# Kernel tuning notes

Measured on AMD Instinct MI355X. Metric: run time of the kernel, lower is better.

## Reference

```python
import jax, jax.numpy as jnp
import numpy as np
from jax import lax

N, CIN, COUT, T, V, G, K = 32, 64, 64, 256, 25, 8, 3  # batch, channels, time, joints, groups, subsets
EPS = 1e-5  # BatchNorm eps


def setup_inputs() -> dict:
    key = jax.random.key(0)
    ks = jax.random.split(key, 10)
    x = jax.random.normal(ks[0], (N, CIN, T, V), jnp.float32)
    # DecoupleA param: A reshaped [3,1,V,V] tiled over groups (torch .repeat tiles)
    A0 = jax.random.uniform(ks[1], (K, 1, V, V), jnp.float32)
    DecoupleA = jnp.tile(A0, (1, G, 1, 1))
    W = jax.random.normal(ks[2], (CIN, COUT * K), jnp.float32) * np.float32(np.sqrt(0.5 / (COUT * K)))
    b = jnp.full((1, COUT * K, 1, 1), 1e-6, jnp.float32)
    g0 = 1.0 + 0.1 * jax.random.normal(ks[3], (COUT * K,), jnp.float32)
    b0 = 0.1 * jax.random.normal(ks[4], (COUT * K,), jnp.float32)
    g1 = 1.0 + 0.1 * jax.random.normal(ks[5], (COUT,), jnp.float32)
    b1 = 0.1 * jax.random.normal(ks[6], (COUT,), jnp.float32)
    conv_w = jax.random.normal(ks[7], (COUT, COUT, 9, 1), jnp.float32) * np.float32(np.sqrt(2.0 / (COUT * 9)))
    conv_b = jnp.zeros((COUT,), jnp.float32)
    g2 = 1.0 + 0.1 * jax.random.normal(ks[8], (COUT,), jnp.float32)
    b2 = 0.1 * jax.random.normal(ks[9], (COUT,), jnp.float32)
    return {"x": x, "DecoupleA": DecoupleA, "W": W, "b": b, "g0": g0, "b0": b0,
            "g1": g1, "b1": b1, "conv_w": conv_w, "conv_b": conv_b, "g2": g2, "b2": b2,
            "keep_prob": 1}


def _bn_eval(y, g, be):
    # inference BN with running_mean=0, running_var=1
    return y * (g / jnp.sqrt(1.0 + EPS))[None, :, None, None] + be[None, :, None, None]


def reference(x, DecoupleA, W, b, g0, b0, g1, b1, conv_w, conv_b, g2, b2, keep_prob):
    # ---- unit_gcn ----
    learn_A = jnp.tile(DecoupleA, (1, COUT // G, 1, 1))           # [3, COUT, V, V]
    # norm(): right-multiply by diag((colsum + 0.001)^-1) == scale columns
    invD = 1.0 / (jnp.sum(learn_A, axis=2) + 0.001)               # [3, COUT, V]
    normA = learn_A * invD[:, :, None, :]
    y = jnp.einsum('nctw,cd->ndtw', x, W) + b                     # [N, 3*COUT, T, V]
    y = _bn_eval(y, g0, b0)
    y = y.reshape(N, K, COUT, T, V)
    y = jnp.einsum('nkctv,kcvw->nctw', y, normA)                  # message passing
    y = _bn_eval(y, g1, b1)
    y = jax.nn.relu(y + x)                                        # down = identity (CIN==COUT)
    # ---- unit_tcn (keep_prob==1 -> DropBlocks are identity) ----
    z = lax.conv_general_dilated(y, conv_w, (1, 1), [(4, 4), (0, 0)],
                                 dimension_numbers=('NCHW', 'OIHW', 'NCHW'))
    z = z + conv_b[None, :, None, None]
    z = _bn_eval(z, g2, b2)
    # ---- residual (identity, CIN==COUT, stride=1; skip-DropBlocks identity) ----
    return jax.nn.relu(z + x)
```

## Files before the change

### kernel.cpp

```cpp
#include <hip/hip_runtime.h>
#include <hip/hip_bf16.h>
#include <stdint.h>


typedef const float* fp;
typedef __attribute__((ext_vector_type(8))) short short8;
typedef __attribute__((ext_vector_type(4))) float floatx4;

__device__ __forceinline__ float us2f(unsigned int u){
  union { unsigned int i; float f; } c; c.i = u << 16; return c.f;
}
__device__ __forceinline__ unsigned short f2us(float f){
  __hip_bfloat16 h = __float2bfloat16(f);
  return *reinterpret_cast<unsigned short*>(&h);
}
__device__ __forceinline__ void gload_lds16(const void* g, void* l){
  __builtin_amdgcn_global_load_lds(
      (const __attribute__((address_space(1))) void*)g,
      (__attribute__((address_space(3))) void*)l, 16, 0, 0);
}


__global__ __launch_bounds__(256) void k_prep(
    fp x, fp A, fp W, fp b, fp g0, fp b0, fp g1, fp b1,
    fp cw, fp cb, fp g2, fp b2,
    unsigned short* U, float* biasU, unsigned short* xb,
    float* cbe, unsigned short* cwetb)
{
  int bid = blockIdx.x, tid = threadIdx.x;
  const float inv_s = rsqrtf(1.0f + 1e-5f);
  __shared__ __align__(16) char smemraw[26624];

  if (bid < 1792) {
    int m = bid;
    if (m >= 1600) {
      for (int k = tid; k < 1600; k += 256) U[(long long)m*1600 + k] = 0;
      return;
    }
    float* nAL   = (float*)smemraw;
    float* WeffL = (float*)(smemraw + 512);
    float* cs3   = (float*)(smemraw + 1408);
    int c = m & 63, w = m >> 6, g = c & 7;
    if (tid < 75) {
      int kk = tid / 25, vv = tid % 25;
      nAL[tid] = A[((kk*8 + g)*25 + vv)*25 + w];
    }
    if (tid < 192) {
      int kk = tid >> 6, cin = tid & 63;
      WeffL[tid] = W[cin*192 + kk*64 + c] * (g0[kk*64 + c] * inv_s);
    }
    __syncthreads();
    if (tid < 3) {
      float s = 0.f;
      for (int vv = 0; vv < 25; vv++) s += nAL[tid*25 + vv];
      cs3[tid] = s + 0.001f;
    }
    __syncthreads();
    if (tid < 75) nAL[tid] = nAL[tid] / cs3[tid/25];
    __syncthreads();
    float s1 = g1[c] * inv_s;
    for (int k = tid; k < 1600; k += 256) {
      int cin = k / 25, vv = k - cin*25;
      float acc = WeffL[cin]       * nAL[vv]
                + WeffL[64 + cin]  * nAL[25 + vv]
                + WeffL[128 + cin] * nAL[50 + vv];
      acc *= s1;
      if (cin == c && vv == w) acc += 1.0f;
      U[(long long)m*1600 + k] = f2us(acc);
    }
    if (tid == 0) {
      float acc = 0.f;
      for (int kk = 0; kk < 3; kk++) {
        int d = kk*64 + c;
        float be = b[d] * (g0[d] * inv_s) + b0[d];
        for (int v = 0; v < 25; v++) acc += be * nAL[kk*25 + v];
      }
      biasU[m] = acc * s1 + b1[c];
    }
    return;
  }

  if (bid < 2816) {
    int bxt = bid - 1792;
    int n = bxt >> 5, tb = bxt & 31, t0 = tb*8;
    unsigned short* xs = (unsigned short*)smemraw;
    for (int e4 = tid; e4 < 3200; e4 += 256) {
      int c = e4 / 50, r4 = (e4 - c*50)*4;
      floatx4 xv = *(const floatx4*)(x + (long long)(n*64 + c)*6400 + t0*25 + r4);
      int tt = r4 / 25, v = r4 - tt*25;
      xs[(c*8 + tt)*26 + v] = f2us(xv.x); if (++v == 25){v = 0; tt++;}
      xs[(c*8 + tt)*26 + v] = f2us(xv.y); if (++v == 25){v = 0; tt++;}
      xs[(c*8 + tt)*26 + v] = f2us(xv.z); if (++v == 25){v = 0; tt++;}
      xs[(c*8 + tt)*26 + v] = f2us(xv.w);
    }
    __syncthreads();
    for (int e4 = tid; e4 < 3200; e4 += 256) {
      int base = e4 * 4;
      int tt = base / 1600, q0 = base - tt*1600;
      int c = q0 / 25, v = q0 - c*25;
      ushort4 pk;
      pk.x = xs[(c*8 + tt)*26 + v]; if (++v == 25){v = 0; c++;}
      pk.y = xs[(c*8 + tt)*26 + v]; if (++v == 25){v = 0; c++;}
      pk.z = xs[(c*8 + tt)*26 + v]; if (++v == 25){v = 0; c++;}
      pk.w = xs[(c*8 + tt)*26 + v];
      *(ushort4*)(xb + (long long)(n*256 + t0 + tt)*1600 + q0) = pk;
    }
    return;
  }

  int gid = (bid - 2816)*256 + tid;
  if (gid < 36864) {
    int o = gid / 576, r = gid % 576;
    int j = r / 64, i = r % 64;
    cwetb[gid] = f2us(cw[(o*64+i)*9 + j] * (g2[o] * inv_s));
    return;
  }
  gid -= 36864;
  if (gid < 64) {
    cbe[gid] = cb[gid] * (g2[gid] * inv_s) + b2[gid];
  }
}

__global__ __launch_bounds__(256, 2) void k_gemm(
    const unsigned short* U, const unsigned short* xb, const float* biasU,
    unsigned short* yb)
{
  int bm = blockIdx.x >> 6, bn = blockIdx.x & 63;
  int n = bn >> 1, t0 = (bn & 1) * 128;
  int tid = threadIdx.x, lane = tid & 63, wid = tid >> 6;
  int l15 = lane & 15, grp = lane >> 4;

  __shared__ __align__(16) unsigned short As[256*64];
  __shared__ __align__(16) unsigned short Bs[128*64];

  const unsigned short* gA[8];
  const unsigned short* gB[4];
  unsigned short* lA[8];
  unsigned short* lB[4];
  #pragma unroll
  for (int it = 0; it < 8; it++) {
    int e = it*256 + tid;
    int row = e >> 3, li = e & 7;
    int kcol = (li ^ (row & 7)) * 8;
    gA[it] = U + (long long)(bm*256 + row)*1600 + kcol;
    lA[it] = As + e*8;
  }
  #pragma unroll
  for (int it = 0; it < 4; it++) {
    int e = it*256 + tid;
    int row = e >> 3, li = e & 7;
    int kcol = (li ^ (row & 7)) * 8;
    gB[it] = xb + (long long)(n*256 + t0 + row)*1600 + kcol;
    lB[it] = Bs + e*8;
  }

  floatx4 acc[4][8];
  #pragma unroll
  for (int i = 0; i < 4; i++)
    #pragma unroll
    for (int j = 0; j < 8; j++) acc[i][j] = (floatx4){0.f,0.f,0.f,0.f};

  for (int kc = 0; kc < 25; kc++) {
    #pragma unroll
    for (int it = 0; it < 8; it++) gload_lds16(gA[it] + kc*64, lA[it]);
    #pragma unroll
    for (int it = 0; it < 4; it++) gload_lds16(gB[it] + kc*64, lB[it]);
    __syncthreads();
    #pragma unroll
    for (int ks = 0; ks < 2; ks++) {
      int colk = ((ks*4 + grp) ^ (l15 & 7)) * 8;
      short8 af[4], bf[8];
      #pragma unroll
      for (int i = 0; i < 4; i++)
        af[i] = *(const short8*)(As + (wid*64 + i*16 + l15)*64 + colk);
      #pragma unroll
      for (int j = 0; j < 8; j++)
        bf[j] = *(const short8*)(Bs + (j*16 + l15)*64 + colk);
      #pragma unroll
      for (int i = 0; i < 4; i++)
        #pragma unroll
        for (int j = 0; j < 8; j++)
          acc[i][j] = __builtin_amdgcn_mfma_f32_16x16x32_bf16(af[i], bf[j], acc[i][j], 0, 0, 0);
    }
    __syncthreads();
  }

  #pragma unroll
  for (int i = 0; i < 4; i++) {
    int mbase = bm*256 + wid*64 + i*16 + grp*4;
    if (mbase >= 1600) continue;
    float4 bu = *(const float4*)(biasU + mbase);
    #pragma unroll
    for (int j = 0; j < 8; j++) {
      int col = j*16 + l15;
      int t = t0 + col;
      ushort4 pk;
      pk.x = f2us(fmaxf(acc[i][j][0] + bu.x, 0.f));
      pk.y = f2us(fmaxf(acc[i][j][1] + bu.y, 0.f));
      pk.z = f2us(fmaxf(acc[i][j][2] + bu.z, 0.f));
      pk.w = f2us(fmaxf(acc[i][j][3] + bu.w, 0.f));
      *(ushort4*)(yb + (long long)(n*256 + t)*1600 + mbase) = pk;
    }
  }
}

__global__ __launch_bounds__(512) void k_tcn(
    const unsigned short* yb, const unsigned short* cwetb, const float* cbe,
    fp x, const unsigned short* zpg, float* out)
{
  int n = blockIdx.x >> 4, tb = blockIdx.x & 15, t0 = tb*16;
  int tid = threadIdx.x, lane = tid & 63, wid = tid >> 6;
  int l15 = lane & 15, grp = lane >> 4;
  __shared__ __align__(16) unsigned short ys[5120*8];

  #pragma unroll
  for (int it = 0; it < 10; it++) {
    int e = it*512 + tid;
    int row = e >> 3, li = e & 7;
    int rt = row / 25, v = row - rt*25;
    int tg = t0 - 4 + rt;
    int sli = li ^ (row & 7);
    bool ok = (row < 600) && (tg >= 0) && (tg < 256);
    const unsigned short* src = ok
      ? yb + ((long long)(n*256 + tg)*1600 + v*64 + sli*8)
      : zpg + li*8;
    gload_lds16(src, ys + e*8);
  }

  int p = wid & 3, h = wid >> 2;
  int o0 = p * 16;
  int o = o0 + l15;
  short8 af[9][2];
  #pragma unroll
  for (int j = 0; j < 9; j++) {
    af[j][0] = *(const short8*)(cwetb + ((o*9 + j)*64 + grp*8));
    af[j][1] = *(const short8*)(cwetb + ((o*9 + j)*64 + 32 + grp*8));
  }
  float4 cb4 = *(const float4*)(cbe + o0 + grp*4);
  __syncthreads();

  for (int tile = h; tile < 25; tile += 2) {
    int colb = tile*16 + l15;
    floatx4 accA = (floatx4){0.f,0.f,0.f,0.f};
    floatx4 accB = (floatx4){0.f,0.f,0.f,0.f};
    #pragma unroll
    for (int j = 0; j < 9; j++) {
      int row = colb + 25*j;
      int r7 = row & 7;
      const unsigned short* rb = ys + row*64;
      short8 b0 = *(const short8*)(rb + ((grp     ^ r7))*8);
      short8 b1 = *(const short8*)(rb + (((4+grp) ^ r7))*8);
      if (j & 1) {
        accB = __builtin_amdgcn_mfma_f32_16x16x32_bf16(af[j][0], b0, accB, 0, 0, 0);
        accB = __builtin_amdgcn_mfma_f32_16x16x32_bf16(af[j][1], b1, accB, 0, 0, 0);
      } else {
        accA = __builtin_amdgcn_mfma_f32_16x16x32_bf16(af[j][0], b0, accA, 0, 0, 0);
        accA = __builtin_amdgcn_mfma_f32_16x16x32_bf16(af[j][1], b1, accA, 0, 0, 0);
      }
    }
    if (colb < 400) {
      int tt = colb / 25, v = colb - tt*25, t = t0 + tt;
      #pragma unroll
      for (int r = 0; r < 4; r++) {
        int oo = o0 + grp*4 + r;
        float val = accA[r] + accB[r] + ((const float*)&cb4)[r]
                  + x[((n*64 + oo)*256 + t)*25 + v];
        out[((n*64 + oo)*256 + t)*25 + v] = fmaxf(val, 0.f);
      }
    }
  }
}

extern "C" void kernel_launch(void* const* d_in, const int* in_sizes, int n_in,
                              void* d_out, int out_size, void* d_ws, size_t ws_size,
                              hipStream_t stream)
{
  fp x  = (fp)d_in[0];
  fp A  = (fp)d_in[1];
  fp W  = (fp)d_in[2];
  fp b  = (fp)d_in[3];
  fp g0 = (fp)d_in[4];
  fp b0 = (fp)d_in[5];
  fp g1 = (fp)d_in[6];
  fp b1 = (fp)d_in[7];
  fp cw = (fp)d_in[8];
  fp cb = (fp)d_in[9];
  fp g2 = (fp)d_in[10];
  fp b2 = (fp)d_in[11];

  char* ws = (char*)d_ws;
  float*          cbe   = (float*)(ws + 117504);
  unsigned short* cwetb = (unsigned short*)(ws + 117760);
  float*          biasU = (float*)(ws + 191488);
  unsigned short* U     = (unsigned short*)(ws + 197888);
  unsigned short* xb    = (unsigned short*)(ws + 5932288);
  unsigned short* yb    = (unsigned short*)(ws + 32146688);
  const unsigned short* zpg = U + (long long)1600*1600;

  k_prep<<<2961, 256, 0, stream>>>(x, A, W, b, g0, b0, g1, b1, cw, cb, g2, b2,
                                   U, biasU, xb, cbe, cwetb);
  k_gemm<<<448, 256, 0, stream>>>(U, xb, biasU, yb);
  k_tcn<<<512, 512, 0, stream>>>(yb, cwetb, cbe, x, zpg, (float*)d_out);
}
```

Before: 210.5 us.

## Split TCN LDS staging in two phases and vectorize prep U writes

The temporal-conv kernel now issues the first 6 of 10 global-to-LDS load batches, then waits only for those. It computes the tiles whose rows fit in that part while the remaining batches load, with a second barrier before the rest of the tiles. The aim is to hide LDS staging latency behind MFMA work, at the cost of an extra barrier and a split tile schedule. In the prep kernel, the x-transpose blocks now come first. The U matrix rows and their zero padding are written as 16-byte short8 stores by 200 threads instead of scalar stores.

```diff
diff --git a/kernel.cpp b/kernel.cpp
--- a/kernel.cpp
+++ b/kernel.cpp
@@ -31,58 +31,8 @@
   const float inv_s = rsqrtf(1.0f + 1e-5f);
   __shared__ __align__(16) char smemraw[26624];
 
-  if (bid < 1792) {
-    int m = bid;
-    if (m >= 1600) {
-      for (int k = tid; k < 1600; k += 256) U[(long long)m*1600 + k] = 0;
-      return;
-    }
-    float* nAL   = (float*)smemraw;
-    float* WeffL = (float*)(smemraw + 512);
-    float* cs3   = (float*)(smemraw + 1408);
-    int c = m & 63, w = m >> 6, g = c & 7;
-    if (tid < 75) {
-      int kk = tid / 25, vv = tid % 25;
-      nAL[tid] = A[((kk*8 + g)*25 + vv)*25 + w];
-    }
-    if (tid < 192) {
-      int kk = tid >> 6, cin = tid & 63;
-      WeffL[tid] = W[cin*192 + kk*64 + c] * (g0[kk*64 + c] * inv_s);
-    }
-    __syncthreads();
-    if (tid < 3) {
-      float s = 0.f;
-      for (int vv = 0; vv < 25; vv++) s += nAL[tid*25 + vv];
-      cs3[tid] = s + 0.001f;
-    }
-    __syncthreads();
-    if (tid < 75) nAL[tid] = nAL[tid] / cs3[tid/25];
-    __syncthreads();
-    float s1 = g1[c] * inv_s;
-    for (int k = tid; k < 1600; k += 256) {
-      int cin = k / 25, vv = k - cin*25;
-      float acc = WeffL[cin]       * nAL[vv]
-                + WeffL[64 + cin]  * nAL[25 + vv]
-                + WeffL[128 + cin] * nAL[50 + vv];
-      acc *= s1;
-      if (cin == c && vv == w) acc += 1.0f;
-      U[(long long)m*1600 + k] = f2us(acc);
-    }
-    if (tid == 0) {
-      float acc = 0.f;
-      for (int kk = 0; kk < 3; kk++) {
-        int d = kk*64 + c;
-        float be = b[d] * (g0[d] * inv_s) + b0[d];
-        for (int v = 0; v < 25; v++) acc += be * nAL[kk*25 + v];
-      }
-      biasU[m] = acc * s1 + b1[c];
-    }
-    return;
-  }
-
-  if (bid < 2816) {
-    int bxt = bid - 1792;
-    int n = bxt >> 5, tb = bxt & 31, t0 = tb*8;
+  if (bid < 1024) {
+    int n = bid >> 5, tb = bid & 31, t0 = tb*8;
     unsigned short* xs = (unsigned short*)smemraw;
     for (int e4 = tid; e4 < 3200; e4 += 256) {
       int c = e4 / 50, r4 = (e4 - c*50)*4;
@@ -108,6 +58,65 @@
     return;
   }
 
+  if (bid < 2816) {
+    int m = bid - 1024;
+    if (m >= 1600) {
+      if (tid < 200) {
+        short8 z = (short8){0,0,0,0,0,0,0,0};
+        *(short8*)(U + (long long)m*1600 + tid*8) = z;
+      }
+      return;
+    }
+    float* nAL   = (float*)smemraw;
+    float* WeffL = (float*)(smemraw + 512);
+    float* cs3   = (float*)(smemraw + 1408);
+    int c = m & 63, w = m >> 6, g = c & 7;
+    if (tid < 75) {
+      int kk = tid / 25, vv = tid % 25;
+      nAL[tid] = A[((kk*8 + g)*25 + vv)*25 + w];
+    }
+    if (tid < 192) {
+      int kk = tid >> 6, cin = tid & 63;
+      WeffL[tid] = W[cin*192 + kk*64 + c] * (g0[kk*64 + c] * inv_s);
+    }
+    __syncthreads();
+    if (tid < 3) {
+      float s = 0.f;
+      for (int vv = 0; vv < 25; vv++) s += nAL[tid*25 + vv];
+      cs3[tid] = s + 0.001f;
+    }
+    __syncthreads();
+    if (tid < 75) nAL[tid] = nAL[tid] / cs3[tid/25];
+    __syncthreads();
+    float s1 = g1[c] * inv_s;
+    if (tid < 200) {
+      int k0 = tid * 8;
+      short8 pk;
+      #pragma unroll
+      for (int q = 0; q < 8; q++) {
+        int k = k0 + q;
+        int cin = k / 25, vv = k - cin*25;
+        float acc = WeffL[cin]       * nAL[vv]
+                  + WeffL[64 + cin]  * nAL[25 + vv]
+                  + WeffL[128 + cin] * nAL[50 + vv];
+        acc *= s1;
+        if (cin == c && vv == w) acc += 1.0f;
+        pk[q] = (short)f2us(acc);
+      }
+      *(short8*)(U + (long long)m*1600 + k0) = pk;
+    }
+    if (tid == 0) {
+      float acc = 0.f;
+      for (int kk = 0; kk < 3; kk++) {
+        int d = kk*64 + c;
+        float be = b[d] * (g0[d] * inv_s) + b0[d];
+        for (int v = 0; v < 25; v++) acc += be * nAL[kk*25 + v];
+      }
+      biasU[m] = acc * s1 + b1[c];
+    }
+    return;
+  }
+
   int gid = (bid - 2816)*256 + tid;
   if (gid < 36864) {
     int o = gid / 576, r = gid % 576;
@@ -214,7 +223,33 @@
   __shared__ __align__(16) unsigned short ys[5120*8];
 
   #pragma unroll
-  for (int it = 0; it < 10; it++) {
+  for (int it = 0; it < 6; it++) {
+    int e = it*512 + tid;
+    int row = e >> 3, li = e & 7;
+    int rt = row / 25, v = row - rt*25;
+    int tg = t0 - 4 + rt;
+    int sli = li ^ (row & 7);
+    bool ok = (tg >= 0) && (tg < 256);
+    const unsigned short* src = ok
+      ? yb + ((long long)(n*256 + tg)*1600 + v*64 + sli*8)
+      : zpg + li*8;
+    gload_lds16(src, ys + e*8);
+  }
+
+  int p = wid & 3, h = wid >> 2;
+  int o0 = p * 16;
+  int o = o0 + l15;
+  short8 af[9][2];
+  #pragma unroll
+  for (int j = 0; j < 9; j++) {
+    af[j][0] = *(const short8*)(cwetb + ((o*9 + j)*64 + grp*8));
+    af[j][1] = *(const short8*)(cwetb + ((o*9 + j)*64 + 32 + grp*8));
+  }
+  float4 cb4 = *(const float4*)(cbe + o0 + grp*4);
+  __syncthreads();
+
+  #pragma unroll
+  for (int it = 6; it < 10; it++) {
     int e = it*512 + tid;
     int row = e >> 3, li = e & 7;
     int rt = row / 25, v = row - rt*25;
@@ -227,47 +262,41 @@
     gload_lds16(src, ys + e*8);
   }
 
-  int p = wid & 3, h = wid >> 2;
-  int o0 = p * 16;
-  int o = o0 + l15;
-  short8 af[9][2];
-  #pragma unroll
-  for (int j = 0; j < 9; j++) {
-    af[j][0] = *(const short8*)(cwetb + ((o*9 + j)*64 + grp*8));
-    af[j][1] = *(const short8*)(cwetb + ((o*9 + j)*64 + 32 + grp*8));
-  }
-  float4 cb4 = *(const float4*)(cbe + o0 + grp*4);
-  __syncthreads();
-
-  for (int tile = h; tile < 25; tile += 2) {
-    int colb = tile*16 + l15;
-    floatx4 accA = (floatx4){0.f,0.f,0.f,0.f};
-    floatx4 accB = (floatx4){0.f,0.f,0.f,0.f};
-    #pragma unroll
-    for (int j = 0; j < 9; j++) {
-      int row = colb + 25*j;
-      int r7 = row & 7;
-      const unsigned short* rb = ys + row*64;
-      short8 b0 = *(const short8*)(rb + ((grp     ^ r7))*8);
-      short8 b1 = *(const short8*)(rb + (((4+grp) ^ r7))*8);
-      if (j & 1) {
-        accB = __builtin_amdgcn_mfma_f32_16x16x32_bf16(af[j][0], b0, accB, 0, 0, 0);
-        accB = __builtin_amdgcn_mfma_f32_16x16x32_bf16(af[j][1], b1, accB, 0, 0, 0);
-      } else {
-        accA = __builtin_amdgcn_mfma_f32_16x16x32_bf16(af[j][0], b0, accA, 0, 0, 0);
-        accA = __builtin_amdgcn_mfma_f32_16x16x32_bf16(af[j][1], b1, accA, 0, 0, 0);
-      }
-    }
-    if (colb < 400) {
-      int tt = colb / 25, v = colb - tt*25, t = t0 + tt;
-      #pragma unroll
-      for (int r = 0; r < 4; r++) {
-        int oo = o0 + grp*4 + r;
-        float val = accA[r] + accB[r] + ((const float*)&cb4)[r]
-                  + x[((n*64 + oo)*256 + t)*25 + v];
-        out[((n*64 + oo)*256 + t)*25 + v] = fmaxf(val, 0.f);
-      }
-    }
+  #pragma unroll 1
+  for (int phase = 0; phase < 2; phase++) {
+    int tstart = phase ? (12 - h) : h;
+    int tend   = phase ? 25 : 11;
+    for (int tile = tstart; tile < tend; tile += 2) {
+      int colb = tile*16 + l15;
+      floatx4 accA = (floatx4){0.f,0.f,0.f,0.f};
+      floatx4 accB = (floatx4){0.f,0.f,0.f,0.f};
+      #pragma unroll
+      for (int j = 0; j < 9; j++) {
+        int row = colb + 25*j;
+        int r7 = row & 7;
+        const unsigned short* rb = ys + row*64;
+        short8 b0 = *(const short8*)(rb + ((grp     ^ r7))*8);
+        short8 b1 = *(const short8*)(rb + (((4+grp) ^ r7))*8);
+        if (j & 1) {
+          accB = __builtin_amdgcn_mfma_f32_16x16x32_bf16(af[j][0], b0, accB, 0, 0, 0);
+          accB = __builtin_amdgcn_mfma_f32_16x16x32_bf16(af[j][1], b1, accB, 0, 0, 0);
+        } else {
+          accA = __builtin_amdgcn_mfma_f32_16x16x32_bf16(af[j][0], b0, accA, 0, 0, 0);
+          accA = __builtin_amdgcn_mfma_f32_16x16x32_bf16(af[j][1], b1, accA, 0, 0, 0);
+        }
+      }
+      if (colb < 400) {
+        int tt = colb / 25, v = colb - tt*25, t = t0 + tt;
+        #pragma unroll
+        for (int r = 0; r < 4; r++) {
+          int oo = o0 + grp*4 + r;
+          float val = accA[r] + accB[r] + ((const float*)&cb4)[r]
+                    + x[((n*64 + oo)*256 + t)*25 + v];
+          out[((n*64 + oo)*256 + t)*25 + v] = fmaxf(val, 0.f);
+        }
+      }
+    }
+    if (phase == 0) __syncthreads();
   }
 }
 
```

Result: no change. 209.6 us (-0.5%).
